# Performance work log

Hardware: AMD Instinct MI355X
Metric: run time of the kernel (lower is better)

## Reference

```python
import jax, jax.numpy as jnp
import numpy as np

N, M, H, R, F = 50000, 64, 128, 4, 7   # nodes, latent, hidden, rounds, node features
E = 800_000                             # directed edges
B, NMAX = 32, 512                       # dense-batch graphs, padded nodes per graph


def setup_inputs() -> dict:
    key = jax.random.key(0)
    ks = jax.random.split(key, 10)
    glorot = lambda k, shape, fan_in: (jax.random.normal(k, shape, jnp.float32)
                                       / np.float32(np.sqrt(fan_in)))
    return {
        "z": jax.random.normal(ks[0], (N, M), jnp.float32),
        "edge_index": jax.random.randint(ks[1], (2, E), 0, N, dtype=jnp.int32),
        "z_dense": jax.random.normal(ks[2], (B, NMAX, M), jnp.float32),
        "bias": jnp.zeros((1,), jnp.float32),
        "W_in": glorot(ks[3], (M, H), M), "b_in": jnp.zeros((H,), jnp.float32),
        "W_msg": glorot(ks[4], (R, H, H), H), "b_msg": jnp.zeros((R, H), jnp.float32),
        "W_upd": glorot(ks[5], (R, H, H), H), "b_upd": jnp.zeros((R, H), jnp.float32),
        "W_out": glorot(ks[6], (H, F), H), "b_out": jnp.zeros((F,), jnp.float32),
    }


def reference(z, edge_index, z_dense, bias, W_in, b_in, W_msg, b_msg,
              W_upd, b_upd, W_out, b_out):
    # decode_edges: (B, n_max, M) -> (B, n_max, n_max) inner-product logits + bias
    edge_logits = jnp.einsum("bnm,bkm->bnk", z_dense, z_dense) + bias[0]

    # decode_nodes: gather -> MLP -> scatter message passing
    src, dst = edge_index[0], edge_index[1]
    num_nodes = z.shape[0]
    state = jax.nn.relu(z @ W_in + b_in)                      # (N, H)
    for r in range(W_msg.shape[0]):                           # R small, fixed
        message = jax.nn.relu(state @ W_msg[r] + b_msg[r])    # (N, H)
        # aggregated[v] = sum_{(u->v) in E} message[u]
        aggregated = jax.ops.segment_sum(message[src], dst, num_segments=num_nodes)
        state = state + jax.nn.relu(aggregated @ W_upd[r] + b_upd[r])
    node_logits = state @ W_out + b_out                       # (N, F)

    return edge_logits, node_logits
```

## Files before the change

### kernel.cpp

```cpp
#include <hip/hip_runtime.h>
#include <cstdint>

#define NN  50000
#define MD  64
#define HD  128
#define RR  4
#define FD  7
#define EE  800000
#define BG  32
#define NMX 512

typedef __attribute__((ext_vector_type(8))) short bf16x8;
typedef __attribute__((ext_vector_type(4))) float f32x4;

__device__ __forceinline__ unsigned short f2bf(float f) {
    unsigned u = __builtin_bit_cast(unsigned, f);
    u = (u + 0x7fffu + ((u >> 16) & 1u)) >> 16;
    return (unsigned short)u;
}
__device__ __forceinline__ float bflo(unsigned u) { return __builtin_bit_cast(float, u << 16); }
__device__ __forceinline__ float bfhi(unsigned u) { return __builtin_bit_cast(float, u & 0xffff0000u); }

__device__ __forceinline__ bf16x8 pack8(float4 a, float4 b) {
    bf16x8 r;
    r[0]=(short)f2bf(a.x); r[1]=(short)f2bf(a.y); r[2]=(short)f2bf(a.z); r[3]=(short)f2bf(a.w);
    r[4]=(short)f2bf(b.x); r[5]=(short)f2bf(b.y); r[6]=(short)f2bf(b.z); r[7]=(short)f2bf(b.w);
    return r;
}

__global__ __launch_bounds__(256) void edge_kernel(const unsigned short* __restrict__ zdb,
                                                   const float* __restrict__ bias,
                                                   float* __restrict__ out) {
    __shared__ float cstage[64][68];
    const int b  = blockIdx.z;
    const int tn = blockIdx.y * 64;
    const int tk = blockIdx.x * 64;
    const unsigned short* zb = zdb + (size_t)b * NMX * MD;
    const int tid = threadIdx.x, wave = tid >> 6, lane = tid & 63;
    const int l15 = lane & 15, k8 = (lane >> 4) * 8;

    const unsigned short* ap = zb + (size_t)(tn + wave * 16 + l15) * MD + k8;
    bf16x8 af0 = *(const bf16x8*)ap;
    bf16x8 af1 = *(const bf16x8*)(ap + 32);

    f32x4 acc[4];
    #pragma unroll
    for (int ct = 0; ct < 4; ct++) acc[ct] = (f32x4){0.f, 0.f, 0.f, 0.f};
    const unsigned short* bp = zb + (size_t)(tk + l15) * MD + k8;
    #pragma unroll
    for (int ct = 0; ct < 4; ct++) {
        bf16x8 b0 = *(const bf16x8*)(bp + (size_t)ct * 16 * MD);
        bf16x8 b1 = *(const bf16x8*)(bp + (size_t)ct * 16 * MD + 32);
        acc[ct] = __builtin_amdgcn_mfma_f32_16x16x32_bf16(af0, b0, acc[ct], 0, 0, 0);
        acc[ct] = __builtin_amdgcn_mfma_f32_16x16x32_bf16(af1, b1, acc[ct], 0, 0, 0);
    }
    #pragma unroll
    for (int ct = 0; ct < 4; ct++)
        #pragma unroll
        for (int i = 0; i < 4; i++)
            cstage[wave * 16 + (lane >> 4) * 4 + i][ct * 16 + l15] = acc[ct][i];
    __syncthreads();
    const float bi = bias[0];
    #pragma unroll
    for (int it = 0; it < 4; it++) {
        int f = tid + it * 256;
        int row = f >> 4, c4 = (f & 15) * 4;
        float4 v = *(const float4*)&cstage[row][c4];
        v.x += bi; v.y += bi; v.z += bi; v.w += bi;
        *(float4*)(out + ((size_t)b * NMX + tn + row) * NMX + tk + c4) = v;
    }
}

__global__ __launch_bounds__(256) void cvt_kernel(const float* __restrict__ src,
                                                  unsigned short* __restrict__ dst,
                                                  int n4) {
    int i = blockIdx.x * 256 + threadIdx.x;
    if (i >= n4) return;
    float4 v = *(const float4*)(src + (size_t)i * 4);
    ushort4 o = {f2bf(v.x), f2bf(v.y), f2bf(v.z), f2bf(v.w)};
    *(ushort4*)(dst + (size_t)i * 4) = o;
}

__global__ __launch_bounds__(256) void tcvt_kernel(const float* __restrict__ src,
                                                   unsigned short* __restrict__ dst,
                                                   int K, int H) {
    int r = blockIdx.y;
    int i = blockIdx.x * 256 + threadIdx.x;
    if (i >= K * H) return;
    int k = i / H, h = i % H;
    float v = src[(size_t)r * K * H + i];
    dst[(size_t)r * K * H + (size_t)h * K + k] = f2bf(v);
}

template <int K1, int MODE>
__global__ __launch_bounds__(256) void fused_kernel(
    const unsigned short* __restrict__ in,
    const unsigned short* __restrict__ Wt1,
    const float* __restrict__ b1,
    float* __restrict__ state,
    const unsigned short* __restrict__ Wt2,
    const float* __restrict__ b2,
    unsigned short* __restrict__ msgb,
    const float* __restrict__ Wout,
    const float* __restrict__ bout,
    float* __restrict__ node_out,
    int nrows)
{
    constexpr int KC1 = K1 / 32;
    __shared__ float cstage[64][132];
    __shared__ float sWout[MODE == 2 ? HD * FD : 1];
    const int tid = threadIdx.x, wave = tid >> 6, lane = tid & 63;
    const int l15 = lane & 15, k8 = (lane >> 4) * 8;
    const int rbase = blockIdx.x * 64;

    if constexpr (MODE == 2)
        for (int i = tid; i < HD * FD; i += 256) sWout[i] = Wout[i];

    int rclamp = min(rbase + wave * 16 + l15, nrows - 1);
    bf16x8 af[KC1];
    #pragma unroll
    for (int c = 0; c < KC1; c++)
        af[c] = *(const bf16x8*)(in + (size_t)rclamp * K1 + (size_t)c * 32 + k8);
    f32x4 acc[8];
    #pragma unroll
    for (int ct = 0; ct < 8; ct++) acc[ct] = (f32x4){0.f, 0.f, 0.f, 0.f};
    const unsigned short* bp = Wt1 + (size_t)l15 * K1 + k8;
    #pragma unroll
    for (int ct = 0; ct < 8; ct++)
        #pragma unroll
        for (int c = 0; c < KC1; c++) {
            bf16x8 bf = *(const bf16x8*)(bp + (size_t)ct * 16 * K1 + c * 32);
            acc[ct] = __builtin_amdgcn_mfma_f32_16x16x32_bf16(af[c], bf, acc[ct], 0, 0, 0);
        }
    #pragma unroll
    for (int ct = 0; ct < 8; ct++)
        #pragma unroll
        for (int i = 0; i < 4; i++)
            cstage[wave * 16 + (lane >> 4) * 4 + i][ct * 16 + l15] = acc[ct][i];
    __syncthreads();

    #pragma unroll
    for (int it = 0; it < 8; it++) {
        int f = tid + it * 256;
        int row = f >> 5, c4 = (f & 31) * 4;
        int grow = rbase + row;
        if (grow < nrows) {
            float4 v = *(const float4*)&cstage[row][c4];
            float4 bb = *(const float4*)(b1 + c4);
            v.x = fmaxf(v.x + bb.x, 0.f);
            v.y = fmaxf(v.y + bb.y, 0.f);
            v.z = fmaxf(v.z + bb.z, 0.f);
            v.w = fmaxf(v.w + bb.w, 0.f);
            if constexpr (MODE >= 1) {
                float4 so = *(const float4*)(state + (size_t)grow * HD + c4);
                v.x += so.x; v.y += so.y; v.z += so.z; v.w += so.w;
            }
            if constexpr (MODE <= 1)
                *(float4*)(state + (size_t)grow * HD + c4) = v;
            *(float4*)&cstage[row][c4] = v;
        }
    }
    __syncthreads();

    if constexpr (MODE <= 1) {
        bf16x8 af2[4];
        #pragma unroll
        for (int c = 0; c < 4; c++) {
            float4 u0 = *(const float4*)&cstage[wave * 16 + l15][c * 32 + k8];
            float4 u1 = *(const float4*)&cstage[wave * 16 + l15][c * 32 + k8 + 4];
            af2[c] = pack8(u0, u1);
        }
        f32x4 acc2[8];
        #pragma unroll
        for (int ct = 0; ct < 8; ct++) acc2[ct] = (f32x4){0.f, 0.f, 0.f, 0.f};
        const unsigned short* bp2 = Wt2 + (size_t)l15 * HD + k8;
        #pragma unroll
        for (int ct = 0; ct < 8; ct++)
            #pragma unroll
            for (int c = 0; c < 4; c++) {
                bf16x8 bf = *(const bf16x8*)(bp2 + (size_t)ct * 16 * HD + c * 32);
                acc2[ct] = __builtin_amdgcn_mfma_f32_16x16x32_bf16(af2[c], bf, acc2[ct], 0, 0, 0);
            }
        __syncthreads();
        #pragma unroll
        for (int ct = 0; ct < 8; ct++)
            #pragma unroll
            for (int i = 0; i < 4; i++)
                cstage[wave * 16 + (lane >> 4) * 4 + i][ct * 16 + l15] = acc2[ct][i];
        __syncthreads();
        #pragma unroll
        for (int it = 0; it < 8; it++) {
            int f = tid + it * 256;
            int row = f >> 5, c4 = (f & 31) * 4;
            int grow = rbase + row;
            if (grow < nrows) {
                float4 v = *(const float4*)&cstage[row][c4];
                float4 bb = *(const float4*)(b2 + c4);
                v.x = fmaxf(v.x + bb.x, 0.f);
                v.y = fmaxf(v.y + bb.y, 0.f);
                v.z = fmaxf(v.z + bb.z, 0.f);
                v.w = fmaxf(v.w + bb.w, 0.f);
                ushort4 o = {f2bf(v.x), f2bf(v.y), f2bf(v.z), f2bf(v.w)};
                *(ushort4*)(msgb + (size_t)grow * HD + c4) = o;
            }
        }
    } else {
        for (int i = tid; i < 64 * FD; i += 256) {
            int row = i / FD, ff = i - row * FD;
            int grow = rbase + row;
            if (grow < nrows) {
                float a = bout[ff];
                #pragma unroll 8
                for (int k = 0; k < HD; k++)
                    a += cstage[row][k] * sWout[k * FD + ff];
                node_out[(size_t)grow * FD + ff] = a;
            }
        }
    }
}

__global__ __launch_bounds__(256) void hist_kernel(const int* __restrict__ dst,
                                                   int* __restrict__ cnt) {
    int e = blockIdx.x * 256 + threadIdx.x;
    if (e < EE) atomicAdd(&cnt[dst[e]], 1);
}

__global__ __launch_bounds__(256) void scan1_kernel(const int* __restrict__ cnt,
                                                    int* __restrict__ incl,
                                                    int* __restrict__ bsum) {
    __shared__ int s[256];
    int i = blockIdx.x * 256 + threadIdx.x;
    int t = threadIdx.x;
    s[t] = (i < NN) ? cnt[i] : 0;
    __syncthreads();
    #pragma unroll
    for (int off = 1; off < 256; off <<= 1) {
        int x = (t >= off) ? s[t - off] : 0;
        __syncthreads();
        s[t] += x;
        __syncthreads();
    }
    if (i < NN) incl[i] = s[t];
    if (t == 255) bsum[blockIdx.x] = s[255];
}

__global__ __launch_bounds__(256) void scan2_kernel(int* __restrict__ bsum, int nb) {
    __shared__ int s[256];
    int t = threadIdx.x;
    int orig = (t < nb) ? bsum[t] : 0;
    s[t] = orig;
    __syncthreads();
    #pragma unroll
    for (int off = 1; off < 256; off <<= 1) {
        int x = (t >= off) ? s[t - off] : 0;
        __syncthreads();
        s[t] += x;
        __syncthreads();
    }
    if (t < nb) bsum[t] = s[t] - orig;
}

__global__ __launch_bounds__(256) void scan3_kernel(const int* __restrict__ cnt,
                                                    const int* __restrict__ incl,
                                                    const int* __restrict__ bsum,
                                                    int* __restrict__ row_ptr,
                                                    int* __restrict__ cursor) {
    int i = blockIdx.x * 256 + threadIdx.x;
    if (i < NN) {
        int ex = incl[i] - cnt[i] + bsum[blockIdx.x];
        row_ptr[i] = ex;
        cursor[i]  = ex;
        if (i == 0) row_ptr[NN] = EE;
    }
}

__global__ __launch_bounds__(256) void bucket_kernel(const int* __restrict__ src,
                                                     const int* __restrict__ dst,
                                                     int* __restrict__ cursor,
                                                     int* __restrict__ colsrc) {
    int e = blockIdx.x * 256 + threadIdx.x;
    if (e < EE) {
        int pos = atomicAdd(&cursor[dst[e]], 1);
        colsrc[pos] = src[e];
    }
}

__global__ __launch_bounds__(256) void gather_kernel(const int* __restrict__ rp,
                                                     const int* __restrict__ colsrc,
                                                     const uint4* __restrict__ msg4,
                                                     uint4* __restrict__ agg4) {
    int v = blockIdx.x * 4 + (threadIdx.x >> 6);
    if (v >= NN) return;
    const int lane = threadIdx.x & 63;
    const int e = lane >> 4, q = lane & 15;
    const int beg = rp[v], end = rp[v + 1];
    float a[8];
    #pragma unroll
    for (int i = 0; i < 8; i++) a[i] = 0.f;

    int j = beg;
    for (; j + 7 < end; j += 8) {
        int c0 = colsrc[j + e];
        int c1 = colsrc[j + 4 + e];
        uint4 u = msg4[(size_t)c0 * 16 + q];
        uint4 w = msg4[(size_t)c1 * 16 + q];
        a[0] += bflo(u.x); a[1] += bfhi(u.x);
        a[2] += bflo(u.y); a[3] += bfhi(u.y);
        a[4] += bflo(u.z); a[5] += bfhi(u.z);
        a[6] += bflo(u.w); a[7] += bfhi(u.w);
        a[0] += bflo(w.x); a[1] += bfhi(w.x);
        a[2] += bflo(w.y); a[3] += bfhi(w.y);
        a[4] += bflo(w.z); a[5] += bfhi(w.z);
        a[6] += bflo(w.w); a[7] += bfhi(w.w);
    }
    for (; j < end; j += 4) {
        if (j + e < end) {
            uint4 u = msg4[(size_t)colsrc[j + e] * 16 + q];
            a[0] += bflo(u.x); a[1] += bfhi(u.x);
            a[2] += bflo(u.y); a[3] += bfhi(u.y);
            a[4] += bflo(u.z); a[5] += bfhi(u.z);
            a[6] += bflo(u.w); a[7] += bfhi(u.w);
        }
    }
    #pragma unroll
    for (int i = 0; i < 8; i++) {
        a[i] += __shfl_xor(a[i], 16);
        a[i] += __shfl_xor(a[i], 32);
    }
    if (lane < 16) {
        uint4 o;
        o.x = (unsigned)f2bf(a[0]) | ((unsigned)f2bf(a[1]) << 16);
        o.y = (unsigned)f2bf(a[2]) | ((unsigned)f2bf(a[3]) << 16);
        o.z = (unsigned)f2bf(a[4]) | ((unsigned)f2bf(a[5]) << 16);
        o.w = (unsigned)f2bf(a[6]) | ((unsigned)f2bf(a[7]) << 16);
        agg4[(size_t)v * 16 + q] = o;
    }
}

extern "C" void kernel_launch(void* const* d_in, const int* in_sizes, int n_in,
                              void* d_out, int out_size, void* d_ws, size_t ws_size,
                              hipStream_t stream) {
    const float* z          = (const float*)d_in[0];
    const int*   edge_index = (const int*)  d_in[1];
    const float* z_dense    = (const float*)d_in[2];
    const float* bias       = (const float*)d_in[3];
    const float* W_in       = (const float*)d_in[4];
    const float* b_in       = (const float*)d_in[5];
    const float* W_msg      = (const float*)d_in[6];
    const float* b_msg      = (const float*)d_in[7];
    const float* W_upd      = (const float*)d_in[8];
    const float* b_upd      = (const float*)d_in[9];
    const float* W_out      = (const float*)d_in[10];
    const float* b_out      = (const float*)d_in[11];

    float* out      = (float*)d_out;
    float* edge_out = out;
    float* node_out = out + (size_t)BG * NMX * NMX;

    char* p = (char*)d_ws;
    float* state = (float*)p;                     p += (size_t)NN * HD * 4;
    unsigned short* msgb   = (unsigned short*)p;  p += (size_t)NN * HD * 2;
    unsigned short* aggb   = (unsigned short*)p;  p += (size_t)NN * HD * 2;
    unsigned short* zb     = (unsigned short*)p;  p += (size_t)NN * MD * 2;
    unsigned short* zdb    = (unsigned short*)p;  p += (size_t)BG * NMX * MD * 2;
    unsigned short* wt_in  = (unsigned short*)p;  p += (size_t)HD * MD * 2;
    unsigned short* wt_msg = (unsigned short*)p;  p += (size_t)RR * HD * HD * 2;
    unsigned short* wt_upd = (unsigned short*)p;  p += (size_t)RR * HD * HD * 2;
    int* cnt     = (int*)p;                       p += (size_t)NN * 4;
    int* incl    = (int*)p;                       p += (size_t)NN * 4;
    int* row_ptr = (int*)p;                       p += (size_t)(NN + 1) * 4;
    int* colsrc  = (int*)p;                       p += (size_t)EE * 4;
    int* bsum    = (int*)p;

    const int* src = edge_index;
    const int* dst = edge_index + EE;
    const int NB = (NN + 255) / 256;
    const int EB = (EE + 255) / 256;

    cvt_kernel<<<(BG * NMX * MD / 4 + 255) / 256, 256, 0, stream>>>(
        z_dense, zdb, BG * NMX * MD / 4);
    dim3 eg(NMX / 64, NMX / 64, BG);
    edge_kernel<<<eg, 256, 0, stream>>>(zdb, bias, edge_out);

    cvt_kernel<<<(NN * MD / 4 + 255) / 256, 256, 0, stream>>>(z, zb, NN * MD / 4);
    tcvt_kernel<<<dim3((MD * HD + 255) / 256, 1), 256, 0, stream>>>(W_in, wt_in, MD, HD);
    tcvt_kernel<<<dim3((HD * HD + 255) / 256, RR), 256, 0, stream>>>(W_msg, wt_msg, HD, HD);
    tcvt_kernel<<<dim3((HD * HD + 255) / 256, RR), 256, 0, stream>>>(W_upd, wt_upd, HD, HD);

    hipMemsetAsync(cnt, 0, NN * sizeof(int), stream);
    hist_kernel<<<EB, 256, 0, stream>>>(dst, cnt);
    scan1_kernel<<<NB, 256, 0, stream>>>(cnt, incl, bsum);
    scan2_kernel<<<1, 256, 0, stream>>>(bsum, NB);
    scan3_kernel<<<NB, 256, 0, stream>>>(cnt, incl, bsum, row_ptr, cnt);
    bucket_kernel<<<EB, 256, 0, stream>>>(src, dst, cnt, colsrc);

    const int MG = (NN + 63) / 64;
    const int GG = (NN + 3) / 4;

    fused_kernel<MD, 0><<<MG, 256, 0, stream>>>(
        zb, wt_in, b_in, state,
        wt_msg, b_msg, msgb, nullptr, nullptr, nullptr, NN);

    for (int r = 0; r < RR - 1; r++) {
        gather_kernel<<<GG, 256, 0, stream>>>(row_ptr, colsrc,
                                              (const uint4*)msgb, (uint4*)aggb);
        fused_kernel<HD, 1><<<MG, 256, 0, stream>>>(
            aggb, wt_upd + (size_t)r * HD * HD, b_upd + (size_t)r * HD, state,
            wt_msg + (size_t)(r + 1) * HD * HD, b_msg + (size_t)(r + 1) * HD,
            msgb, nullptr, nullptr, nullptr, NN);
    }
    gather_kernel<<<GG, 256, 0, stream>>>(row_ptr, colsrc,
                                          (const uint4*)msgb, (uint4*)aggb);
    fused_kernel<HD, 2><<<MG, 256, 0, stream>>>(
        aggb, wt_upd + (size_t)(RR - 1) * HD * HD, b_upd + (size_t)(RR - 1) * HD, state,
        nullptr, nullptr, nullptr, W_out, b_out, node_out, NN);
}
```

Before: 417.9 us.

## Build CSR with two-pass LDS-atomic radix bucketing instead of global atomics

Replaces the global-atomic histogram and bucket scatter used to build the destination-sorted CSR with a two-pass radix partition. Pass one buckets edges by dst>>8 using per-block shared-memory histograms and cursors. Pass two sorts each 256-node bucket locally in LDS and writes row_ptr and colsrc. This removes contended global atomics and the memset, at the cost of an extra 8-byte-per-edge intermediate buffer. With only 196 blocks per pass, the GPU may be underoccupied.

```diff
diff --git a/kernel.cpp b/kernel.cpp
--- a/kernel.cpp
+++ b/kernel.cpp
@@ -9,6 +9,12 @@
 #define EE  800000
 #define BG  32
 #define NMX 512
+
+#define NH   196
+#define NBL  196
+#define BE   4096
+#define NS   (NH * NBL)
+#define NSB  ((NS + 255) / 256)
 
 typedef __attribute__((ext_vector_type(8))) short bf16x8;
 typedef __attribute__((ext_vector_type(4))) float f32x4;
@@ -219,19 +225,28 @@
     }
 }
 
-__global__ __launch_bounds__(256) void hist_kernel(const int* __restrict__ dst,
-                                                   int* __restrict__ cnt) {
-    int e = blockIdx.x * 256 + threadIdx.x;
-    if (e < EE) atomicAdd(&cnt[dst[e]], 1);
-}
-
-__global__ __launch_bounds__(256) void scan1_kernel(const int* __restrict__ cnt,
+__global__ __launch_bounds__(256) void p1c_kernel(const int* __restrict__ dst,
+                                                  int* __restrict__ bh) {
+    __shared__ int h[NH];
+    const int b = blockIdx.x;
+    for (int i = threadIdx.x; i < NH; i += 256) h[i] = 0;
+    __syncthreads();
+    const int e0 = b * BE;
+    for (int i = threadIdx.x; i < BE; i += 256) {
+        int e = e0 + i;
+        if (e < EE) atomicAdd(&h[dst[e] >> 8], 1);
+    }
+    __syncthreads();
+    for (int i = threadIdx.x; i < NH; i += 256) bh[i * NBL + b] = h[i];
+}
+
+__global__ __launch_bounds__(256) void scan1_kernel(const int* __restrict__ in,
                                                     int* __restrict__ incl,
-                                                    int* __restrict__ bsum) {
+                                                    int* __restrict__ bsum, int n) {
     __shared__ int s[256];
     int i = blockIdx.x * 256 + threadIdx.x;
     int t = threadIdx.x;
-    s[t] = (i < NN) ? cnt[i] : 0;
+    s[t] = (i < n) ? in[i] : 0;
     __syncthreads();
     #pragma unroll
     for (int off = 1; off < 256; off <<= 1) {
@@ -240,7 +255,7 @@
         s[t] += x;
         __syncthreads();
     }
-    if (i < NN) incl[i] = s[t];
+    if (i < n) incl[i] = s[t];
     if (t == 255) bsum[blockIdx.x] = s[255];
 }
 
@@ -260,28 +275,69 @@
     if (t < nb) bsum[t] = s[t] - orig;
 }
 
-__global__ __launch_bounds__(256) void scan3_kernel(const int* __restrict__ cnt,
-                                                    const int* __restrict__ incl,
-                                                    const int* __restrict__ bsum,
-                                                    int* __restrict__ row_ptr,
-                                                    int* __restrict__ cursor) {
+__global__ __launch_bounds__(256) void scanex_kernel(const int* __restrict__ in,
+                                                     const int* __restrict__ incl,
+                                                     const int* __restrict__ bsum,
+                                                     int* __restrict__ ex, int n) {
     int i = blockIdx.x * 256 + threadIdx.x;
-    if (i < NN) {
-        int ex = incl[i] - cnt[i] + bsum[blockIdx.x];
-        row_ptr[i] = ex;
-        cursor[i]  = ex;
-        if (i == 0) row_ptr[NN] = EE;
-    }
-}
-
-__global__ __launch_bounds__(256) void bucket_kernel(const int* __restrict__ src,
-                                                     const int* __restrict__ dst,
-                                                     int* __restrict__ cursor,
-                                                     int* __restrict__ colsrc) {
-    int e = blockIdx.x * 256 + threadIdx.x;
-    if (e < EE) {
-        int pos = atomicAdd(&cursor[dst[e]], 1);
-        colsrc[pos] = src[e];
+    if (i < n) ex[i] = incl[i] - in[i] + bsum[blockIdx.x];
+}
+
+__global__ __launch_bounds__(256) void p1s_kernel(const int* __restrict__ src,
+                                                  const int* __restrict__ dst,
+                                                  const int* __restrict__ ex,
+                                                  int2* __restrict__ sorted) {
+    __shared__ int cur[NH];
+    const int b = blockIdx.x;
+    for (int i = threadIdx.x; i < NH; i += 256) cur[i] = ex[i * NBL + b];
+    __syncthreads();
+    const int e0 = b * BE;
+    for (int i = threadIdx.x; i < BE; i += 256) {
+        int e = e0 + i;
+        if (e < EE) {
+            int d = dst[e];
+            int pos = atomicAdd(&cur[d >> 8], 1);
+            sorted[pos] = make_int2(d, src[e]);
+        }
+    }
+}
+
+__global__ __launch_bounds__(256) void p2_kernel(const int2* __restrict__ sorted,
+                                                 const int* __restrict__ ex,
+                                                 int* __restrict__ row_ptr,
+                                                 int* __restrict__ colsrc) {
+    __shared__ int hist[256];
+    __shared__ int scanb[256];
+    __shared__ int cur[256];
+    const int h = blockIdx.x;
+    const int t = threadIdx.x;
+    const int base = ex[h * NBL];
+    const int endp = (h == NH - 1) ? EE : ex[(h + 1) * NBL];
+    const int cnt  = endp - base;
+    hist[t] = 0;
+    __syncthreads();
+    for (int i = t; i < cnt; i += 256)
+        atomicAdd(&hist[sorted[base + i].x & 255], 1);
+    __syncthreads();
+    scanb[t] = hist[t];
+    __syncthreads();
+    #pragma unroll
+    for (int off = 1; off < 256; off <<= 1) {
+        int x = (t >= off) ? scanb[t - off] : 0;
+        __syncthreads();
+        scanb[t] += x;
+        __syncthreads();
+    }
+    int excl = scanb[t] - hist[t];
+    cur[t] = excl;
+    int v = h * 256 + t;
+    if (v < NN) row_ptr[v] = base + excl;
+    if (h == NH - 1 && t == 0) row_ptr[NN] = EE;
+    __syncthreads();
+    for (int i = t; i < cnt; i += 256) {
+        int2 pr = sorted[base + i];
+        int pos = base + atomicAdd(&cur[pr.x & 255], 1);
+        colsrc[pos] = pr.y;
     }
 }
 
@@ -366,16 +422,16 @@
     unsigned short* wt_in  = (unsigned short*)p;  p += (size_t)HD * MD * 2;
     unsigned short* wt_msg = (unsigned short*)p;  p += (size_t)RR * HD * HD * 2;
     unsigned short* wt_upd = (unsigned short*)p;  p += (size_t)RR * HD * HD * 2;
-    int* cnt     = (int*)p;                       p += (size_t)NN * 4;
-    int* incl    = (int*)p;                       p += (size_t)NN * 4;
-    int* row_ptr = (int*)p;                       p += (size_t)(NN + 1) * 4;
-    int* colsrc  = (int*)p;                       p += (size_t)EE * 4;
-    int* bsum    = (int*)p;
+    int*  bh      = (int*)p;                      p += (size_t)NS * 4;
+    int*  incl    = (int*)p;                      p += (size_t)NS * 4;
+    int*  exsc    = (int*)p;                      p += (size_t)NS * 4;
+    int*  row_ptr = (int*)p;                      p += (size_t)(NN + 1) * 4;
+    int*  colsrc  = (int*)p;                      p += (size_t)EE * 4;
+    int2* sorted  = (int2*)p;                     p += (size_t)EE * 8;
+    int*  bsum    = (int*)p;
 
     const int* src = edge_index;
     const int* dst = edge_index + EE;
-    const int NB = (NN + 255) / 256;
-    const int EB = (EE + 255) / 256;
 
     cvt_kernel<<<(BG * NMX * MD / 4 + 255) / 256, 256, 0, stream>>>(
         z_dense, zdb, BG * NMX * MD / 4);
@@ -387,12 +443,12 @@
     tcvt_kernel<<<dim3((HD * HD + 255) / 256, RR), 256, 0, stream>>>(W_msg, wt_msg, HD, HD);
     tcvt_kernel<<<dim3((HD * HD + 255) / 256, RR), 256, 0, stream>>>(W_upd, wt_upd, HD, HD);
 
-    hipMemsetAsync(cnt, 0, NN * sizeof(int), stream);
-    hist_kernel<<<EB, 256, 0, stream>>>(dst, cnt);
-    scan1_kernel<<<NB, 256, 0, stream>>>(cnt, incl, bsum);
-    scan2_kernel<<<1, 256, 0, stream>>>(bsum, NB);
-    scan3_kernel<<<NB, 256, 0, stream>>>(cnt, incl, bsum, row_ptr, cnt);
-    bucket_kernel<<<EB, 256, 0, stream>>>(src, dst, cnt, colsrc);
+    p1c_kernel<<<NBL, 256, 0, stream>>>(dst, bh);
+    scan1_kernel<<<NSB, 256, 0, stream>>>(bh, incl, bsum, NS);
+    scan2_kernel<<<1, 256, 0, stream>>>(bsum, NSB);
+    scanex_kernel<<<NSB, 256, 0, stream>>>(bh, incl, bsum, exsc, NS);
+    p1s_kernel<<<NBL, 256, 0, stream>>>(src, dst, exsc, sorted);
+    p2_kernel<<<NH, 256, 0, stream>>>(sorted, exsc, row_ptr, colsrc);
 
     const int MG = (NN + 63) / 64;
     const int GG = (NN + 3) / 4;
```

After: 359.6 us. 1.16x faster.
